# Performance work log

Hardware: AMD Instinct MI355X
Metric: run time of the kernel (lower is better)

The kernel has to match this reference:

```python
import jax, jax.numpy as jnp
import numpy as np

EMBED_DIM = 512
NUM_HEADS = 8
HEAD_DIM = EMBED_DIM // NUM_HEADS
REL_MAX = 16
NUM_POS_IDS = 2 * REL_MAX + 1 + 1  # 34 (directed + padding id)
PADDING_IDX = 0
B, S = 2, 2048


def setup_inputs() -> dict:
    key = jax.random.key(0)
    ks = jax.random.split(key, 9)
    Q = jax.random.normal(ks[0], (B, S, EMBED_DIM), dtype=jnp.float32)
    K = jax.random.normal(ks[1], (B, S, EMBED_DIM), dtype=jnp.float32)
    V = jax.random.normal(ks[2], (B, S, EMBED_DIM), dtype=jnp.float32)
    rel_pos_ids = jax.random.randint(ks[3], (B, S, S), 0, NUM_POS_IDS, dtype=jnp.int64) if jax.config.jax_enable_x64 else jax.random.randint(ks[3], (B, S, S), 0, NUM_POS_IDS, dtype=jnp.int32)
    scale = 0.02
    Wq = jax.random.normal(ks[4], (EMBED_DIM, EMBED_DIM), dtype=jnp.float32) * scale
    Wk = jax.random.normal(ks[5], (EMBED_DIM, EMBED_DIM), dtype=jnp.float32) * scale
    Wv = jax.random.normal(ks[6], (EMBED_DIM, EMBED_DIM), dtype=jnp.float32) * scale
    Wo = jax.random.normal(ks[7], (EMBED_DIM, EMBED_DIM), dtype=jnp.float32) * scale
    rel_emb = jax.random.normal(ks[8], (NUM_POS_IDS, EMBED_DIM), dtype=jnp.float32) * scale
    rel_emb = rel_emb.at[PADDING_IDX].set(0.0)  # nn.Embedding padding_idx row is zero
    return {"Q": Q, "K": K, "V": V, "rel_pos_ids": rel_pos_ids,
            "Wq": Wq, "Wk": Wk, "Wv": Wv, "Wo": Wo, "rel_emb": rel_emb}


def _proj(x, W):
    # Linear (no bias) then strided head split: view(B, S, head_dim, H) -> (B, H, S, head_dim)
    b, s, _ = x.shape
    y = x @ W.T
    return y.reshape(b, s, HEAD_DIM, NUM_HEADS).transpose(0, 3, 1, 2)


def _forward(Q, K, V, rel_pos_ids, Wq, Wk, Wv, Wo, rel_emb):
    b, sq, _ = Q.shape
    Qp = _proj(Q, Wq)  # (B, H, Sq, hd)
    Kp = _proj(K, Wk)  # (B, H, Sk, hd)
    Vp = _proj(V, Wv)  # (B, H, Sk, hd)

    # rel_embeds split per head with the same strided layout: (P, hd, H) -> (H, P, hd)
    R = rel_emb.reshape(NUM_POS_IDS, HEAD_DIM, NUM_HEADS).transpose(2, 0, 1)
    # Q_rel: (B, H, Sq, P)
    Q_rel = jnp.einsum('bhsd,hpd->bhsp', Qp, R)
    # gather per-pair relative bias: (B, H, Sq, Sk)
    rel_shift = jnp.take_along_axis(Q_rel, rel_pos_ids[:, None, :, :], axis=3)
    mask = (rel_pos_ids == PADDING_IDX)[:, None, :, :]
    rel_shift = jnp.where(mask, -jnp.inf, rel_shift)

    energy = (jnp.einsum('bhqd,bhkd->bhqk', Qp, Kp) + rel_shift) / jnp.sqrt(jnp.float32(HEAD_DIM))
    attn = jax.nn.softmax(energy, axis=-1)
    out = jnp.einsum('bhqk,bhkd->bhqd', attn, Vp)  # (B, H, Sq, hd)
    # inverse of strided split: (B, Sq, hd, H) -> flatten last two
    out = out.transpose(0, 2, 3, 1).reshape(b, sq, EMBED_DIM)
    return out @ Wo.T


def reference(Q, K, V, rel_pos_ids, Wq, Wk, Wv, Wo, rel_emb):
    return _forward(Q, K, V, rel_pos_ids, Wq, Wk, Wv, Wo, rel_emb)
```

## Files before the change

### kernel.cpp

```cpp
#include <hip/hip_runtime.h>
#include <cstdint>
#include <cstddef>

#define SEQ   2048
#define BBAT  2
#define EMBED 512
#define NH    8
#define HD    64
#define NPOS  34

typedef __bf16 bf16;
typedef __bf16 bf16x8 __attribute__((ext_vector_type(8)));
typedef float  f32x4  __attribute__((ext_vector_type(4)));

#define ESCALE 0.1803368801111204f

__device__ __forceinline__ f32x4 mfma16(bf16x8 a, bf16x8 b, f32x4 c){
  return __builtin_amdgcn_mfma_f32_16x16x32_bf16(a, b, c, 0, 0, 0);
}

__global__ __launch_bounds__(256) void k_prep(
    const float* __restrict__ Q, const float* __restrict__ K, const float* __restrict__ V,
    const float* __restrict__ Wq, const float* __restrict__ Wk,
    const float* __restrict__ Wv, const float* __restrict__ Wo,
    const float* __restrict__ RE,
    bf16* __restrict__ Qb, bf16* __restrict__ Kb, bf16* __restrict__ Vb,
    bf16* __restrict__ Wall, bf16* __restrict__ Rb)
{
  const int NCONV = 3*524288;
  const int NW = 196608, NO = 262144;
  int i = blockIdx.x*256 + threadIdx.x;
  if (i < NCONV){
    int tsel = i >> 19, j = i & 524287;
    const float* s = tsel==0 ? Q : (tsel==1 ? K : V);
    bf16* d       = tsel==0 ? Qb : (tsel==1 ? Kb : Vb);
    float4 v = ((const float4*)s)[j];
    union { bf16 e[4]; ushort4 u; } pk;
    pk.e[0]=(bf16)v.x; pk.e[1]=(bf16)v.y; pk.e[2]=(bf16)v.z; pk.e[3]=(bf16)v.w;
    ((ushort4*)d)[j] = pk.u;
  } else {
    int j = i - NCONV;
    if (j < NW){
      int w  = j >> 16;
      int r  = j & 65535;
      int np = r >> 7, c4 = (r & 127) << 2;
      const float* W = (w==0) ? Wq : ((w==1) ? Wk : Wv);
      int src = ((np & 63) << 3) + (np >> 6);
      float4 v = *(const float4*)(W + (size_t)src*512 + c4);
      union { bf16 e[4]; ushort4 u; } pk;
      pk.e[0]=(bf16)v.x; pk.e[1]=(bf16)v.y; pk.e[2]=(bf16)v.z; pk.e[3]=(bf16)v.w;
      *(ushort4*)(Wall + (size_t)w*262144 + (size_t)np*512 + c4) = pk.u;
    } else if (j < NW + NO){
      int jj = j - NW;
      int n = jj >> 9, kp = jj & 511;
      int src = ((kp & 63) << 3) + (kp >> 6);
      Wall[(size_t)3*262144 + (size_t)n*512 + kp] = (bf16)Wo[(size_t)n*512 + src];
    } else {
      int jj = j - NW - NO;
      if (jj < 8*48*64){
        int h  = jj / (48*64);
        int r2 = jj - h*(48*64);
        int p  = r2 >> 6, dd = r2 & 63;
        float v = (p < NPOS) ? RE[(size_t)p*512 + dd*8 + h] : 0.f;
        Rb[jj] = (bf16)v;
      }
    }
  }
}

__global__ __launch_bounds__(256,2) void k_gemm_proj(
    const bf16* __restrict__ Qb, const bf16* __restrict__ Kb, const bf16* __restrict__ Vb,
    const bf16* __restrict__ W,  bf16* __restrict__ Qp, bf16* __restrict__ Kp, bf16* __restrict__ Vt)
{
  const bf16* A  = blockIdx.z==0 ? Qb : (blockIdx.z==1 ? Kb : Vb);
  const bf16* Bw = W + (size_t)blockIdx.z*262144;

  __shared__ __align__(16) bf16 As[128][72];
  __shared__ __align__(16) bf16 Bs[64][72];
  const int t = threadIdx.x;
  const int w = t >> 6, lane = t & 63, l15 = lane & 15, quad = lane >> 4;
  const int wm = (w & 1) * 64, wn = (w >> 1) * 32;
  const int m0 = blockIdx.y * 128, n0 = blockIdx.x * 64;

  f32x4 acc[4][2];
  #pragma unroll
  for (int mt=0; mt<4; ++mt)
    #pragma unroll
    for (int nt=0; nt<2; ++nt) acc[mt][nt] = (f32x4){0.f,0.f,0.f,0.f};

  for (int kt = 0; kt < 512; kt += 64){
    #pragma unroll
    for (int i = 0; i < 4; ++i){
      int lin = t + 256*i;
      int r = lin >> 3, c8 = (lin & 7) << 3;
      *(uint4*)&As[r][c8] = *(const uint4*)(A + (size_t)(m0 + r)*512 + kt + c8);
    }
    #pragma unroll
    for (int i = 0; i < 2; ++i){
      int lin = t + 256*i;
      int r = lin >> 3, c8 = (lin & 7) << 3;
      *(uint4*)&Bs[r][c8] = *(const uint4*)(Bw + (size_t)(n0 + r)*512 + kt + c8);
    }
    __syncthreads();
    #pragma unroll
    for (int ks = 0; ks < 2; ++ks){
      bf16x8 am[4], bn[2];
      #pragma unroll
      for (int x=0;x<4;++x) am[x] = *(const bf16x8*)&As[wm + x*16 + l15][ks*32 + quad*8];
      #pragma unroll
      for (int y=0;y<2;++y) bn[y] = *(const bf16x8*)&Bs[wn + y*16 + l15][ks*32 + quad*8];
      #pragma unroll
      for (int mt=0;mt<4;++mt)
        #pragma unroll
        for (int nt=0;nt<2;++nt)
          acc[mt][nt] = mfma16(am[mt], bn[nt], acc[mt][nt]);
    }
    __syncthreads();
  }

  if (blockIdx.z != 2){
    bf16* C = blockIdx.z==0 ? Qp : Kp;
    #pragma unroll
    for (int mt=0;mt<4;++mt)
      #pragma unroll
      for (int r=0;r<4;++r){
        int m = m0 + wm + mt*16 + quad*4 + r;
        #pragma unroll
        for (int nt=0;nt<2;++nt)
          C[(size_t)m*512 + n0 + wn + nt*16 + l15] = (bf16)acc[mt][nt][r];
      }
  } else {
    bf16 (*VT)[136] = (bf16(*)[136])As;
    #pragma unroll
    for (int mt=0;mt<4;++mt)
      #pragma unroll
      for (int r=0;r<4;++r){
        int m = wm + mt*16 + quad*4 + r;
        #pragma unroll
        for (int nt=0;nt<2;++nt)
          VT[wn + nt*16 + l15][m] = (bf16)acc[mt][nt][r];
      }
    __syncthreads();
    const int h = blockIdx.x, b = m0 >> 11, s0 = m0 & 2047;
    const int n = t >> 2, c0 = (t & 3) * 32;
    bf16* dst = Vt + ((size_t)((b*NH + h)*HD + n))*SEQ + s0 + c0;
    #pragma unroll
    for (int i = 0; i < 4; ++i)
      *(uint4*)(dst + i*8) = *(const uint4*)&VT[n][c0 + i*8];
  }
}

__global__ __launch_bounds__(256,2) void k_gemm_out(
    const bf16* __restrict__ A, const bf16* __restrict__ Bw, float* __restrict__ C)
{
  __shared__ __align__(16) bf16 As[64][72];
  __shared__ __align__(16) bf16 Bs[64][72];
  const int t = threadIdx.x;
  const int w = t >> 6, lane = t & 63, l15 = lane & 15, quad = lane >> 4;
  const int wm = (w & 1) * 32, wn = (w >> 1) * 32;
  const int m0 = blockIdx.y * 64, n0 = blockIdx.x * 64;

  f32x4 acc[2][2];
  #pragma unroll
  for (int mt=0; mt<2; ++mt)
    #pragma unroll
    for (int nt=0; nt<2; ++nt) acc[mt][nt] = (f32x4){0.f,0.f,0.f,0.f};

  for (int kt = 0; kt < 512; kt += 64){
    #pragma unroll
    for (int i = 0; i < 2; ++i){
      int lin = t + 256*i;
      int r = lin >> 3, c8 = (lin & 7) << 3;
      *(uint4*)&As[r][c8] = *(const uint4*)(A  + (size_t)(m0 + r)*512 + kt + c8);
      *(uint4*)&Bs[r][c8] = *(const uint4*)(Bw + (size_t)(n0 + r)*512 + kt + c8);
    }
    __syncthreads();
    #pragma unroll
    for (int ks = 0; ks < 2; ++ks){
      bf16x8 am[2], bn[2];
      #pragma unroll
      for (int x=0;x<2;++x) am[x] = *(const bf16x8*)&As[wm + x*16 + l15][ks*32 + quad*8];
      #pragma unroll
      for (int y=0;y<2;++y) bn[y] = *(const bf16x8*)&Bs[wn + y*16 + l15][ks*32 + quad*8];
      #pragma unroll
      for (int mt=0;mt<2;++mt)
        #pragma unroll
        for (int nt=0;nt<2;++nt)
          acc[mt][nt] = mfma16(am[mt], bn[nt], acc[mt][nt]);
    }
    __syncthreads();
  }
  #pragma unroll
  for (int mt=0;mt<2;++mt)
    #pragma unroll
    for (int r=0;r<4;++r){
      int m = m0 + wm + mt*16 + quad*4 + r;
      #pragma unroll
      for (int nt=0;nt<2;++nt)
        C[(size_t)m*512 + n0 + wn + nt*16 + l15] = acc[mt][nt][r];
    }
}

__global__ __launch_bounds__(256,2) void k_attn(
    const bf16* __restrict__ Qp, const bf16* __restrict__ Kp,
    const bf16* __restrict__ Vt, const bf16* __restrict__ Rb,
    const int* __restrict__ ids, bf16* __restrict__ Out)
{
  __shared__ __align__(16) bf16 Ks[128][72];
  __shared__ __align__(16) bf16 Vs[64][136];
  __shared__ __align__(16) bf16 Ps[64][136];
  __shared__ float lut[64][35];
  __shared__ float lsum_s[128];

  const int t = threadIdx.x;
  const int b = blockIdx.z, h = blockIdx.y;
  const int q0 = blockIdx.x * 64;
  const int w = t >> 6, lane = t & 63, l15 = lane & 15, quad = lane >> 4;
  const int qh = w & 1, kh = w >> 1;

  const size_t idb = (size_t)b*SEQ*SEQ;

  int nid[2][4][4];
  #pragma unroll
  for (int mt=0; mt<2; ++mt)
    #pragma unroll
    for (int nt=0; nt<4; ++nt)
      #pragma unroll
      for (int r=0; r<4; ++r)
        nid[mt][nt][r] = ids[idb + (size_t)(q0 + qh*32 + mt*16 + quad*4 + r)*SEQ
                             + kh*64 + nt*16 + l15];

  {
    const bf16* qbrow = Qp + (size_t)(b*SEQ + q0 + w*16 + l15)*EMBED + h*HD;
    bf16x8 ab0 = *(const bf16x8*)(qbrow + quad*8);
    bf16x8 ab1 = *(const bf16x8*)(qbrow + 32 + quad*8);
    const bf16* rh = Rb + h*3072;
    #pragma unroll
    for (int nt = 0; nt < 3; ++nt){
      bf16x8 r0 = *(const bf16x8*)(rh + (nt*16 + l15)*64 + quad*8);
      bf16x8 r1 = *(const bf16x8*)(rh + (nt*16 + l15)*64 + 32 + quad*8);
      f32x4 c = (f32x4){0.f,0.f,0.f,0.f};
      c = mfma16(ab0, r0, c);
      c = mfma16(ab1, r1, c);
      int p = nt*16 + l15;
      if (p < NPOS){
        #pragma unroll
        for (int r = 0; r < 4; ++r)
          lut[w*16 + quad*4 + r][p] = (p == 0) ? 0.f : exp2f(c[r]*ESCALE);
      }
    }
  }

  bf16x8 aq[2][2];
  #pragma unroll
  for (int mt = 0; mt < 2; ++mt){
    const bf16* qrow = Qp + (size_t)(b*SEQ + q0 + qh*32 + mt*16 + l15)*EMBED + h*HD;
    aq[mt][0] = *(const bf16x8*)(qrow + quad*8);
    aq[mt][1] = *(const bf16x8*)(qrow + 32 + quad*8);
  }

  const bf16* kbase = Kp + (size_t)b*SEQ*EMBED + h*HD;
  const bf16* vbase = Vt + (size_t)(b*NH + h)*HD*SEQ;

  f32x4 acc[2][2];
  #pragma unroll
  for (int mt=0;mt<2;++mt)
    #pragma unroll
    for (int nt=0;nt<2;++nt) acc[mt][nt] = (f32x4){0.f,0.f,0.f,0.f};
  float lsum[2][4] = {{0.f,0.f,0.f,0.f},{0.f,0.f,0.f,0.f}};

  for (int kt = 0; kt < 16; ++kt){
    const int k0 = kt * 128;
    #pragma unroll
    for (int i = 0; i < 4; ++i){
      int lin = t + 256*i;
      int r = lin >> 3, c8 = (lin & 7) << 3;
      *(uint4*)&Ks[r][c8] = *(const uint4*)(kbase + (size_t)(k0 + r)*EMBED + c8);
    }
    #pragma unroll
    for (int i = 0; i < 4; ++i){
      int lin = t + 256*i;
      int d = lin >> 4, c8 = (lin & 15) << 3;
      *(uint4*)&Vs[d][c8] = *(const uint4*)(vbase + (size_t)d*SEQ + k0 + c8);
    }
    __syncthreads();

    float wv[2][4][4];
    #pragma unroll
    for (int mt = 0; mt < 2; ++mt)
      #pragma unroll
      for (int nt = 0; nt < 4; ++nt)
        #pragma unroll
        for (int r = 0; r < 4; ++r)
          wv[mt][nt][r] = lut[qh*32 + mt*16 + quad*4 + r][nid[mt][nt][r]];

    if (kt < 15){
      #pragma unroll
      for (int mt = 0; mt < 2; ++mt)
        #pragma unroll
        for (int nt = 0; nt < 4; ++nt)
          #pragma unroll
          for (int r = 0; r < 4; ++r)
            nid[mt][nt][r] = ids[idb + (size_t)(q0 + qh*32 + mt*16 + quad*4 + r)*SEQ
                                 + (k0 + 128) + kh*64 + nt*16 + l15];
    }

    f32x4 sf[2][4];
    #pragma unroll
    for (int nt = 0; nt < 4; ++nt){
      bf16x8 bk0 = *(const bf16x8*)&Ks[kh*64 + nt*16 + l15][quad*8];
      bf16x8 bk1 = *(const bf16x8*)&Ks[kh*64 + nt*16 + l15][32 + quad*8];
      #pragma unroll
      for (int mt = 0; mt < 2; ++mt){
        f32x4 c = (f32x4){0.f,0.f,0.f,0.f};
        c = mfma16(aq[mt][0], bk0, c);
        c = mfma16(aq[mt][1], bk1, c);
        sf[mt][nt] = c;
      }
    }

    #pragma unroll
    for (int mt = 0; mt < 2; ++mt)
      #pragma unroll
      for (int nt = 0; nt < 4; ++nt)
        #pragma unroll
        for (int r = 0; r < 4; ++r){
          float p = exp2f(sf[mt][nt][r]*ESCALE) * wv[mt][nt][r];
          lsum[mt][r] += p;
          Ps[qh*32 + mt*16 + quad*4 + r][kh*64 + nt*16 + l15] = (bf16)p;
        }
    __syncthreads();

    #pragma unroll
    for (int kk = 0; kk < 4; ++kk){
      bf16x8 ap[2];
      #pragma unroll
      for (int mt = 0; mt < 2; ++mt)
        ap[mt] = *(const bf16x8*)&Ps[qh*32 + mt*16 + l15][kk*32 + quad*8];
      #pragma unroll
      for (int nt = 0; nt < 2; ++nt){
        bf16x8 bv = *(const bf16x8*)&Vs[kh*32 + nt*16 + l15][kk*32 + quad*8];
        #pragma unroll
        for (int mt = 0; mt < 2; ++mt)
          acc[mt][nt] = mfma16(ap[mt], bv, acc[mt][nt]);
      }
    }
    __syncthreads();
  }

  #pragma unroll
  for (int mt = 0; mt < 2; ++mt)
    #pragma unroll
    for (int r = 0; r < 4; ++r){
      float v = lsum[mt][r];
      v += __shfl_xor(v, 1); v += __shfl_xor(v, 2);
      v += __shfl_xor(v, 4); v += __shfl_xor(v, 8);
      if (l15 == 0) lsum_s[kh*64 + qh*32 + mt*16 + quad*4 + r] = v;
    }
  __syncthreads();

  #pragma unroll
  for (int mt = 0; mt < 2; ++mt){
    #pragma unroll
    for (int r = 0; r < 4; ++r){
      int ql = qh*32 + mt*16 + quad*4 + r;
      float inv = 1.f / (lsum_s[ql] + lsum_s[64 + ql]);
      #pragma unroll
      for (int nt = 0; nt < 2; ++nt){
        int d = kh*32 + nt*16 + l15;
        Out[(size_t)(b*SEQ + q0 + ql)*EMBED + h*HD + d] = (bf16)(acc[mt][nt][r]*inv);
      }
    }
  }
}

extern "C" void kernel_launch(void* const* d_in, const int* in_sizes, int n_in,
                              void* d_out, int out_size, void* d_ws, size_t ws_size,
                              hipStream_t stream)
{
  (void)in_sizes; (void)n_in; (void)out_size;
  const float* Q  = (const float*)d_in[0];
  const float* K  = (const float*)d_in[1];
  const float* V  = (const float*)d_in[2];
  const int*   ID = (const int*)d_in[3];
  const float* Wq = (const float*)d_in[4];
  const float* Wk = (const float*)d_in[5];
  const float* Wv = (const float*)d_in[6];
  const float* Wo = (const float*)d_in[7];
  const float* RE = (const float*)d_in[8];
  float* out = (float*)d_out;

  const size_t MB = (size_t)1 << 20;
  if (ws_size < 36*MB) return;
  char* ws = (char*)d_ws;
  bf16*  Qb    = (bf16*)(ws + 0*MB);
  bf16*  Kb    = (bf16*)(ws + 4*MB);
  bf16*  Vb    = (bf16*)(ws + 8*MB);
  bf16*  Qp    = (bf16*)(ws + 12*MB);
  bf16*  Kp    = (bf16*)(ws + 16*MB);
  bf16*  Vt    = (bf16*)(ws + 20*MB);
  bf16*  Wall  = (bf16*)(ws + 24*MB);
  bf16*  Wop   = Wall + (size_t)3*262144;
  bf16*  Rb    = (bf16*)(ws + 26*MB);
  bf16*  AO    = (bf16*)(ws + 0*MB);

  k_prep      <<<dim3(8032),    256, 0, stream>>>(Q, K, V, Wq, Wk, Wv, Wo, RE,
                                                  Qb, Kb, Vb, Wall, Rb);
  k_gemm_proj <<<dim3(8,32,3),  256, 0, stream>>>(Qb, Kb, Vb, Wall, Qp, Kp, Vt);
  k_attn      <<<dim3(32,8,2),  256, 0, stream>>>(Qp, Kp, Vt, Rb, ID, AO);
  k_gemm_out  <<<dim3(8,64),    256, 0, stream>>>(AO, Wop, out);
}
```

Before: 192.9 us.

## Fuse fp32-to-bf16 conversion into GEMMs and drop prep kernel

Removes the separate prep kernel. The projection GEMM now loads fp32 inputs and weights directly, converting them to bf16 in registers with a one-tile register prefetch, and uses a larger 128x128 tile. The Wo permutation/conversion and the rel-embedding gather move into the attention kernel. That kernel also stores its LUT as bf16 and aliases the P buffer over K tiles, which needs an extra barrier, so it can target higher occupancy. The output GEMM gains register prefetching as well. This cuts a launch and a round trip through bf16 intermediates, at the cost of redundant scattered RE loads per block and reduced LUT precision.

```diff
diff --git a/kernel.cpp b/kernel.cpp
--- a/kernel.cpp
+++ b/kernel.cpp
@@ -19,134 +19,103 @@
   return __builtin_amdgcn_mfma_f32_16x16x32_bf16(a, b, c, 0, 0, 0);
 }
 
-__global__ __launch_bounds__(256) void k_prep(
+__global__ __launch_bounds__(256,2) void k_gemm_proj(
     const float* __restrict__ Q, const float* __restrict__ K, const float* __restrict__ V,
-    const float* __restrict__ Wq, const float* __restrict__ Wk,
-    const float* __restrict__ Wv, const float* __restrict__ Wo,
-    const float* __restrict__ RE,
-    bf16* __restrict__ Qb, bf16* __restrict__ Kb, bf16* __restrict__ Vb,
-    bf16* __restrict__ Wall, bf16* __restrict__ Rb)
+    const float* __restrict__ Wq, const float* __restrict__ Wk, const float* __restrict__ Wv,
+    bf16* __restrict__ Qp, bf16* __restrict__ Kp, bf16* __restrict__ Vt)
 {
-  const int NCONV = 3*524288;
-  const int NW = 196608, NO = 262144;
-  int i = blockIdx.x*256 + threadIdx.x;
-  if (i < NCONV){
-    int tsel = i >> 19, j = i & 524287;
-    const float* s = tsel==0 ? Q : (tsel==1 ? K : V);
-    bf16* d       = tsel==0 ? Qb : (tsel==1 ? Kb : Vb);
-    float4 v = ((const float4*)s)[j];
-    union { bf16 e[4]; ushort4 u; } pk;
-    pk.e[0]=(bf16)v.x; pk.e[1]=(bf16)v.y; pk.e[2]=(bf16)v.z; pk.e[3]=(bf16)v.w;
-    ((ushort4*)d)[j] = pk.u;
-  } else {
-    int j = i - NCONV;
-    if (j < NW){
-      int w  = j >> 16;
-      int r  = j & 65535;
-      int np = r >> 7, c4 = (r & 127) << 2;
-      const float* W = (w==0) ? Wq : ((w==1) ? Wk : Wv);
-      int src = ((np & 63) << 3) + (np >> 6);
-      float4 v = *(const float4*)(W + (size_t)src*512 + c4);
-      union { bf16 e[4]; ushort4 u; } pk;
-      pk.e[0]=(bf16)v.x; pk.e[1]=(bf16)v.y; pk.e[2]=(bf16)v.z; pk.e[3]=(bf16)v.w;
-      *(ushort4*)(Wall + (size_t)w*262144 + (size_t)np*512 + c4) = pk.u;
-    } else if (j < NW + NO){
-      int jj = j - NW;
-      int n = jj >> 9, kp = jj & 511;
-      int src = ((kp & 63) << 3) + (kp >> 6);
-      Wall[(size_t)3*262144 + (size_t)n*512 + kp] = (bf16)Wo[(size_t)n*512 + src];
-    } else {
-      int jj = j - NW - NO;
-      if (jj < 8*48*64){
-        int h  = jj / (48*64);
-        int r2 = jj - h*(48*64);
-        int p  = r2 >> 6, dd = r2 & 63;
-        float v = (p < NPOS) ? RE[(size_t)p*512 + dd*8 + h] : 0.f;
-        Rb[jj] = (bf16)v;
-      }
-    }
-  }
-}
-
-__global__ __launch_bounds__(256,2) void k_gemm_proj(
-    const bf16* __restrict__ Qb, const bf16* __restrict__ Kb, const bf16* __restrict__ Vb,
-    const bf16* __restrict__ W,  bf16* __restrict__ Qp, bf16* __restrict__ Kp, bf16* __restrict__ Vt)
-{
-  const bf16* A  = blockIdx.z==0 ? Qb : (blockIdx.z==1 ? Kb : Vb);
-  const bf16* Bw = W + (size_t)blockIdx.z*262144;
-
-  __shared__ __align__(16) bf16 As[128][72];
-  __shared__ __align__(16) bf16 Bs[64][72];
+  __shared__ __align__(16) bf16 smem[18432];
+  bf16 (*As)[72] = (bf16(*)[72])smem;
+  bf16 (*Bs)[72] = (bf16(*)[72])(smem + 9216);
+  const int z = blockIdx.z;
+  const float* A = z==0 ? Q : (z==1 ? K : V);
+  const float* W = z==0 ? Wq : (z==1 ? Wk : Wv);
   const int t = threadIdx.x;
   const int w = t >> 6, lane = t & 63, l15 = lane & 15, quad = lane >> 4;
-  const int wm = (w & 1) * 64, wn = (w >> 1) * 32;
-  const int m0 = blockIdx.y * 128, n0 = blockIdx.x * 64;
-
-  f32x4 acc[4][2];
-  #pragma unroll
-  for (int mt=0; mt<4; ++mt)
-    #pragma unroll
-    for (int nt=0; nt<2; ++nt) acc[mt][nt] = (f32x4){0.f,0.f,0.f,0.f};
+  const int wm = (w & 1) * 64, wn = (w >> 1) * 64;
+  const int m0 = blockIdx.y * 128, n0 = blockIdx.x * 128;
+
+  f32x4 acc[4][4];
+  #pragma unroll
+  for (int mt=0;mt<4;++mt)
+    #pragma unroll
+    for (int nt=0;nt<4;++nt) acc[mt][nt] = (f32x4){0.f,0.f,0.f,0.f};
+
+  float4 pa[8], pb[8];
+  #pragma unroll
+  for (int i=0;i<8;++i){
+    int fl = t + 256*i, row = fl >> 4, c4 = (fl & 15) << 2;
+    pa[i] = *(const float4*)(A + (size_t)(m0 + row)*512 + c4);
+    int src = (((n0 + row) & 63) << 3) + ((n0 + row) >> 6);
+    pb[i] = *(const float4*)(W + (size_t)src*512 + c4);
+  }
 
   for (int kt = 0; kt < 512; kt += 64){
     #pragma unroll
-    for (int i = 0; i < 4; ++i){
-      int lin = t + 256*i;
-      int r = lin >> 3, c8 = (lin & 7) << 3;
-      *(uint4*)&As[r][c8] = *(const uint4*)(A + (size_t)(m0 + r)*512 + kt + c8);
-    }
-    #pragma unroll
-    for (int i = 0; i < 2; ++i){
-      int lin = t + 256*i;
-      int r = lin >> 3, c8 = (lin & 7) << 3;
-      *(uint4*)&Bs[r][c8] = *(const uint4*)(Bw + (size_t)(n0 + r)*512 + kt + c8);
-    }
-    __syncthreads();
+    for (int i=0;i<8;++i){
+      int fl = t + 256*i, row = fl >> 4, c4 = (fl & 15) << 2;
+      union { bf16 e[4]; ushort4 u; } ca, cb;
+      ca.e[0]=(bf16)pa[i].x; ca.e[1]=(bf16)pa[i].y; ca.e[2]=(bf16)pa[i].z; ca.e[3]=(bf16)pa[i].w;
+      cb.e[0]=(bf16)pb[i].x; cb.e[1]=(bf16)pb[i].y; cb.e[2]=(bf16)pb[i].z; cb.e[3]=(bf16)pb[i].w;
+      *(ushort4*)&As[row][c4] = ca.u;
+      *(ushort4*)&Bs[row][c4] = cb.u;
+    }
+    __syncthreads();
+    if (kt < 448){
+      #pragma unroll
+      for (int i=0;i<8;++i){
+        int fl = t + 256*i, row = fl >> 4, c4 = (fl & 15) << 2;
+        pa[i] = *(const float4*)(A + (size_t)(m0 + row)*512 + kt + 64 + c4);
+        int src = (((n0 + row) & 63) << 3) + ((n0 + row) >> 6);
+        pb[i] = *(const float4*)(W + (size_t)src*512 + kt + 64 + c4);
+      }
+    }
     #pragma unroll
     for (int ks = 0; ks < 2; ++ks){
-      bf16x8 am[4], bn[2];
+      bf16x8 am[4], bn[4];
       #pragma unroll
       for (int x=0;x<4;++x) am[x] = *(const bf16x8*)&As[wm + x*16 + l15][ks*32 + quad*8];
       #pragma unroll
-      for (int y=0;y<2;++y) bn[y] = *(const bf16x8*)&Bs[wn + y*16 + l15][ks*32 + quad*8];
+      for (int y=0;y<4;++y) bn[y] = *(const bf16x8*)&Bs[wn + y*16 + l15][ks*32 + quad*8];
       #pragma unroll
       for (int mt=0;mt<4;++mt)
         #pragma unroll
-        for (int nt=0;nt<2;++nt)
+        for (int nt=0;nt<4;++nt)
           acc[mt][nt] = mfma16(am[mt], bn[nt], acc[mt][nt]);
     }
     __syncthreads();
   }
 
-  if (blockIdx.z != 2){
-    bf16* C = blockIdx.z==0 ? Qp : Kp;
+  if (z != 2){
+    bf16* C = z==0 ? Qp : Kp;
     #pragma unroll
     for (int mt=0;mt<4;++mt)
       #pragma unroll
       for (int r=0;r<4;++r){
         int m = m0 + wm + mt*16 + quad*4 + r;
         #pragma unroll
-        for (int nt=0;nt<2;++nt)
+        for (int nt=0;nt<4;++nt)
           C[(size_t)m*512 + n0 + wn + nt*16 + l15] = (bf16)acc[mt][nt][r];
       }
   } else {
-    bf16 (*VT)[136] = (bf16(*)[136])As;
+    bf16 (*VT)[136] = (bf16(*)[136])smem;
     #pragma unroll
     for (int mt=0;mt<4;++mt)
       #pragma unroll
       for (int r=0;r<4;++r){
         int m = wm + mt*16 + quad*4 + r;
         #pragma unroll
-        for (int nt=0;nt<2;++nt)
+        for (int nt=0;nt<4;++nt)
           VT[wn + nt*16 + l15][m] = (bf16)acc[mt][nt][r];
       }
     __syncthreads();
-    const int h = blockIdx.x, b = m0 >> 11, s0 = m0 & 2047;
-    const int n = t >> 2, c0 = (t & 3) * 32;
-    bf16* dst = Vt + ((size_t)((b*NH + h)*HD + n))*SEQ + s0 + c0;
-    #pragma unroll
-    for (int i = 0; i < 4; ++i)
-      *(uint4*)(dst + i*8) = *(const uint4*)&VT[n][c0 + i*8];
+    const int nl = t >> 1, half = t & 1;
+    const int gh = (n0 + nl) >> 6, d = (n0 + nl) & 63;
+    const int b = m0 >> 11, s0 = (m0 & 2047) + half*64;
+    bf16* dst = Vt + ((size_t)((b*NH + gh)*HD + d))*SEQ + s0;
+    #pragma unroll
+    for (int j = 0; j < 8; ++j)
+      *(uint4*)(dst + j*8) = *(const uint4*)&VT[nl][half*64 + j*8];
   }
 }
 
@@ -166,15 +135,30 @@
     #pragma unroll
     for (int nt=0; nt<2; ++nt) acc[mt][nt] = (f32x4){0.f,0.f,0.f,0.f};
 
+  uint4 pa[2], pb[2];
+  #pragma unroll
+  for (int i=0;i<2;++i){
+    int lin = t + 256*i, r = lin >> 3, c8 = (lin & 7) << 3;
+    pa[i] = *(const uint4*)(A  + (size_t)(m0 + r)*512 + c8);
+    pb[i] = *(const uint4*)(Bw + (size_t)(n0 + r)*512 + c8);
+  }
+
   for (int kt = 0; kt < 512; kt += 64){
     #pragma unroll
     for (int i = 0; i < 2; ++i){
-      int lin = t + 256*i;
-      int r = lin >> 3, c8 = (lin & 7) << 3;
-      *(uint4*)&As[r][c8] = *(const uint4*)(A  + (size_t)(m0 + r)*512 + kt + c8);
-      *(uint4*)&Bs[r][c8] = *(const uint4*)(Bw + (size_t)(n0 + r)*512 + kt + c8);
-    }
-    __syncthreads();
+      int lin = t + 256*i, r = lin >> 3, c8 = (lin & 7) << 3;
+      *(uint4*)&As[r][c8] = pa[i];
+      *(uint4*)&Bs[r][c8] = pb[i];
+    }
+    __syncthreads();
+    if (kt < 448){
+      #pragma unroll
+      for (int i = 0; i < 2; ++i){
+        int lin = t + 256*i, r = lin >> 3, c8 = (lin & 7) << 3;
+        pa[i] = *(const uint4*)(A  + (size_t)(m0 + r)*512 + kt + 64 + c8);
+        pb[i] = *(const uint4*)(Bw + (size_t)(n0 + r)*512 + kt + 64 + c8);
+      }
+    }
     #pragma unroll
     for (int ks = 0; ks < 2; ++ks){
       bf16x8 am[2], bn[2];
@@ -201,16 +185,18 @@
     }
 }
 
-__global__ __launch_bounds__(256,2) void k_attn(
+__global__ __launch_bounds__(256,4) void k_attn(
     const bf16* __restrict__ Qp, const bf16* __restrict__ Kp,
-    const bf16* __restrict__ Vt, const bf16* __restrict__ Rb,
-    const int* __restrict__ ids, bf16* __restrict__ Out)
+    const bf16* __restrict__ Vt, const float* __restrict__ RE,
+    const float* __restrict__ Wo, const int* __restrict__ ids,
+    bf16* __restrict__ Out, bf16* __restrict__ Wop)
 {
-  __shared__ __align__(16) bf16 Ks[128][72];
+  __shared__ __align__(16) bf16 KP[9216];
   __shared__ __align__(16) bf16 Vs[64][136];
-  __shared__ __align__(16) bf16 Ps[64][136];
-  __shared__ float lut[64][35];
+  __shared__ bf16 lut[64][36];
   __shared__ float lsum_s[128];
+  bf16 (*Ks)[72]  = (bf16(*)[72])KP;
+  bf16 (*Ps)[136] = (bf16(*)[136])KP;
 
   const int t = threadIdx.x;
   const int b = blockIdx.z, h = blockIdx.y;
@@ -218,6 +204,15 @@
   const int w = t >> 6, lane = t & 63, l15 = lane & 15, quad = lane >> 4;
   const int qh = w & 1, kh = w >> 1;
 
+  {
+    int n = blockIdx.x + 32*blockIdx.y + 256*blockIdx.z;
+    int kp0 = t*2, kp1 = t*2 + 1;
+    int s0i = ((kp0 & 63) << 3) + (kp0 >> 6);
+    int s1i = ((kp1 & 63) << 3) + (kp1 >> 6);
+    Wop[(size_t)n*512 + kp0] = (bf16)Wo[(size_t)n*512 + s0i];
+    Wop[(size_t)n*512 + kp1] = (bf16)Wo[(size_t)n*512 + s1i];
+  }
+
   const size_t idb = (size_t)b*SEQ*SEQ;
 
   int nid[2][4][4];
@@ -234,19 +229,27 @@
     const bf16* qbrow = Qp + (size_t)(b*SEQ + q0 + w*16 + l15)*EMBED + h*HD;
     bf16x8 ab0 = *(const bf16x8*)(qbrow + quad*8);
     bf16x8 ab1 = *(const bf16x8*)(qbrow + 32 + quad*8);
-    const bf16* rh = Rb + h*3072;
     #pragma unroll
     for (int nt = 0; nt < 3; ++nt){
-      bf16x8 r0 = *(const bf16x8*)(rh + (nt*16 + l15)*64 + quad*8);
-      bf16x8 r1 = *(const bf16x8*)(rh + (nt*16 + l15)*64 + 32 + quad*8);
+      int p = nt*16 + l15;
+      bf16x8 r0, r1;
+      if (p < NPOS){
+        #pragma unroll
+        for (int j = 0; j < 8; ++j){
+          r0[j] = (bf16)RE[(size_t)p*512 + (quad*8 + j)*8 + h];
+          r1[j] = (bf16)RE[(size_t)p*512 + (32 + quad*8 + j)*8 + h];
+        }
+      } else {
+        #pragma unroll
+        for (int j = 0; j < 8; ++j){ r0[j] = (bf16)0.f; r1[j] = (bf16)0.f; }
+      }
       f32x4 c = (f32x4){0.f,0.f,0.f,0.f};
       c = mfma16(ab0, r0, c);
       c = mfma16(ab1, r1, c);
-      int p = nt*16 + l15;
       if (p < NPOS){
         #pragma unroll
         for (int r = 0; r < 4; ++r)
-          lut[w*16 + quad*4 + r][p] = (p == 0) ? 0.f : exp2f(c[r]*ESCALE);
+          lut[w*16 + quad*4 + r][p] = (p == 0) ? (bf16)0.f : (bf16)exp2f(c[r]*ESCALE);
       }
     }
   }
@@ -292,7 +295,7 @@
       for (int nt = 0; nt < 4; ++nt)
         #pragma unroll
         for (int r = 0; r < 4; ++r)
-          wv[mt][nt][r] = lut[qh*32 + mt*16 + quad*4 + r][nid[mt][nt][r]];
+          wv[mt][nt][r] = (float)lut[qh*32 + mt*16 + quad*4 + r][nid[mt][nt][r]];
 
     if (kt < 15){
       #pragma unroll
@@ -318,6 +321,7 @@
         sf[mt][nt] = c;
       }
     }
+    __syncthreads();
 
     #pragma unroll
     for (int mt = 0; mt < 2; ++mt)
@@ -393,20 +397,13 @@
   const size_t MB = (size_t)1 << 20;
   if (ws_size < 36*MB) return;
   char* ws = (char*)d_ws;
-  bf16*  Qb    = (bf16*)(ws + 0*MB);
-  bf16*  Kb    = (bf16*)(ws + 4*MB);
-  bf16*  Vb    = (bf16*)(ws + 8*MB);
-  bf16*  Qp    = (bf16*)(ws + 12*MB);
-  bf16*  Kp    = (bf16*)(ws + 16*MB);
-  bf16*  Vt    = (bf16*)(ws + 20*MB);
-  bf16*  Wall  = (bf16*)(ws + 24*MB);
-  bf16*  Wop   = Wall + (size_t)3*262144;
-  bf16*  Rb    = (bf16*)(ws + 26*MB);
-  bf16*  AO    = (bf16*)(ws + 0*MB);
-
-  k_prep      <<<dim3(8032),    256, 0, stream>>>(Q, K, V, Wq, Wk, Wv, Wo, RE,
-                                                  Qb, Kb, Vb, Wall, Rb);
-  k_gemm_proj <<<dim3(8,32,3),  256, 0, stream>>>(Qb, Kb, Vb, Wall, Qp, Kp, Vt);
-  k_attn      <<<dim3(32,8,2),  256, 0, stream>>>(Qp, Kp, Vt, Rb, ID, AO);
-  k_gemm_out  <<<dim3(8,64),    256, 0, stream>>>(AO, Wop, out);
+  bf16* Qp  = (bf16*)(ws + 0*MB);
+  bf16* Kp  = (bf16*)(ws + 4*MB);
+  bf16* Vtw = (bf16*)(ws + 8*MB);
+  bf16* AO  = (bf16*)(ws + 12*MB);
+  bf16* Wop = (bf16*)(ws + 16*MB);
+
+  k_gemm_proj <<<dim3(4,32,3), 256, 0, stream>>>(Q, K, V, Wq, Wk, Wv, Qp, Kp, Vtw);
+  k_attn      <<<dim3(32,8,2), 256, 0, stream>>>(Qp, Kp, Vtw, RE, Wo, ID, AO, Wop);
+  k_gemm_out  <<<dim3(8,64),   256, 0, stream>>>(AO, Wop, out);
 }
```

New measurement: 388.9 us. 102% more time.
